# Optimization experiments

Hardware: AMD Instinct MI355X
Metric: run time of the kernel (lower is better)

## Reference

```python
import jax, jax.numpy as jnp
import numpy as np


def _conv1x1(x, W, b):
    # x: (n, c_in, h, w); W: (c_out, c_in); b: (c_out,)
    return jnp.einsum('nchw,oc->nohw', x, W) + b[None, :, None, None]


def setup_inputs() -> dict:
    key = jax.random.key(0)
    ks = jax.random.split(key, 9)
    n, C, h, w = 2, 256, 64, 64
    Ch = C // 2
    s_in = 0.02
    return {
        'feature': jax.random.normal(ks[0], (n, C, h, w), dtype=jnp.float32),
        'Wq': jax.random.normal(ks[1], (Ch, C), dtype=jnp.float32) * s_in,
        'bq': jax.random.normal(ks[2], (Ch,), dtype=jnp.float32) * s_in,
        'Wk': jax.random.normal(ks[3], (Ch, C), dtype=jnp.float32) * s_in,
        'bk': jax.random.normal(ks[4], (Ch,), dtype=jnp.float32) * s_in,
        'Wv': jax.random.normal(ks[5], (Ch, C), dtype=jnp.float32) * s_in,
        'bv': jax.random.normal(ks[6], (Ch,), dtype=jnp.float32) * s_in,
        'Wm': jax.random.normal(ks[7], (C, Ch), dtype=jnp.float32) * s_in,
        'bm': jax.random.normal(ks[8], (C,), dtype=jnp.float32) * s_in,
    }


def reference(feature, Wq, bq, Wk, bk, Wv, bv, Wm, bm):
    n, C, h, w = feature.shape
    Ch = C // 2
    N = n * h * w
    # 1x1 conv projections, then flatten batch+spatial into one sequence dim
    q = _conv1x1(feature, Wq, bq)  # (n, Ch, h, w)
    k = _conv1x1(feature, Wk, bk)
    v = _conv1x1(feature, Wv, bv)
    # NCHW -> NHWC -> (N, Ch), matching torch transpose(1,2).transpose(2,3).reshape
    q = jnp.transpose(q, (0, 2, 3, 1)).reshape(N, Ch)
    k = jnp.transpose(k, (0, 2, 3, 1)).reshape(N, Ch)
    v = jnp.transpose(v, (0, 2, 3, 1)).reshape(N, Ch)
    # scores = k @ q.T (note: torch code uses k as rows, q.T as cols)
    scores = k @ q.T  # (N, N)
    attn = jax.nn.softmax(scores, axis=-1)
    mask = attn @ v  # (N, Ch)
    mask = mask.reshape(n, h, w, Ch)
    # torch transpose chain (2,3)->(1,2)->(2,3): (n,h,w,Ch) -> (n,Ch,w,h)
    mask = jnp.transpose(mask, (0, 3, 2, 1))
    out = _conv1x1(mask, Wm, bm)  # (n, C, w, h); h==w so residual add is valid
    return out + feature
```

## Files before the change

### kernel.cpp

```cpp
#include <hip/hip_runtime.h>
#include <hip/hip_bf16.h>

#define LOG2E 1.44269504088896340736f

typedef __attribute__((ext_vector_type(8))) short short8;
typedef __attribute__((ext_vector_type(4))) float f32x4;
typedef __attribute__((ext_vector_type(2))) unsigned int uint2v;
typedef __attribute__((ext_vector_type(4))) unsigned int uint4v;
typedef unsigned int u32;

__device__ __forceinline__ short f2bf(float f) {
    unsigned u = __builtin_bit_cast(unsigned, f);
    unsigned r = (u + 0x7FFFu + ((u >> 16) & 1u)) >> 16;
    return (short)r;
}

__device__ __forceinline__ float bf2f(short x) {
    unsigned u = ((unsigned)(unsigned short)x) << 16;
    return __builtin_bit_cast(float, u);
}

__device__ __forceinline__ unsigned cvt_pk_bf16(float lo, float hi) {
    unsigned r;
    asm volatile("v_cvt_pk_bf16_f32 %0, %1, %2" : "=v"(r) : "v"(lo), "v"(hi));
    return r;
}

__device__ __forceinline__ float fexp2(float x) {
    float r;
    asm("v_exp_f32 %0, %1" : "=v"(r) : "v"(x));
    return r;
}

__global__ __launch_bounds__(64) void wprep_kernel(
    const float* __restrict__ Wq, const float* __restrict__ bq,
    const float* __restrict__ Wk, const float* __restrict__ bk,
    const float* __restrict__ Wv, const float* __restrict__ bv,
    const float* __restrict__ Wm,
    short* __restrict__ Wb, float* __restrict__ bqkv, short* __restrict__ Wmb)
{
    const int b = blockIdx.x;
    const int t = threadIdx.x;
    if (b < 384) {
        const int mat = b >> 7, row = b & 127;
        const float* src = (mat == 0 ? Wq : mat == 1 ? Wk : Wv) + (size_t)row * 256;
        const float sc = (mat == 1) ? LOG2E : 1.f;
        float4 v = *(const float4*)(src + t * 4);
        uint2v pk;
        pk.x = cvt_pk_bf16(v.x * sc, v.y * sc);
        pk.y = cvt_pk_bf16(v.z * sc, v.w * sc);
        *(uint2v*)(Wb + (size_t)b * 256 + t * 4) = pk;
    } else if (b == 384) {
        for (int e = t; e < 384; e += 64) {
            const int mat = e >> 7;
            const float* bsrc = (mat == 0 ? bq : mat == 1 ? bk : bv);
            bqkv[e] = bsrc[e & 127] * (mat == 1 ? LOG2E : 1.f);
        }
    } else {
        const int row = b - 385;
        float2 v = *(const float2*)(Wm + (size_t)row * 128 + t * 2);
        *(u32*)(Wmb + (size_t)row * 128 + t * 2) = cvt_pk_bf16(v.x, v.y);
    }
}

__global__ __launch_bounds__(256) void proj_kernel(
    const float* __restrict__ feat, const short* __restrict__ Wb,
    const float* __restrict__ bqkv,
    short* __restrict__ Qb, short* __restrict__ Kb, short* __restrict__ VTg)
{
    __shared__ __align__(16) short Xs[16 * 256];
    __shared__ __align__(16) short VTs[128 * 16];
    const int t = threadIdx.x;
    const int blk = blockIdx.x;
    const int ib = blk * 16;
    const int n = ib >> 12;
    const int hw0 = ib & 4095;

    {
        const int r = t & 15, cg = t >> 4;
        const float* fp = feat + (size_t)n * 1048576 + (size_t)(cg * 16) * 4096 + hw0 + r;
        short8 t0, t1;
        #pragma unroll
        for (int ci = 0; ci < 8; ++ci) {
            t0[ci] = f2bf(fp[(size_t)ci * 4096]);
            t1[ci] = f2bf(fp[(size_t)(ci + 8) * 4096]);
        }
        const int sw = (r & 7) << 2;
        *(short8*)(&Xs[r * 256 + ((cg * 2) ^ sw) * 8]) = t0;
        *(short8*)(&Xs[r * 256 + ((cg * 2 + 1) ^ sw) * 8]) = t1;
    }
    __syncthreads();

    const int lane = t & 63;
    const int w = __builtin_amdgcn_readfirstlane(t >> 6);
    const int l15 = lane & 15;
    const int g = lane >> 4;
    const int o0w = w * 96;

    f32x4 acc[6];
    #pragma unroll
    for (int osub = 0; osub < 6; ++osub)
        acc[osub] = *(const f32x4*)(bqkv + o0w + osub * 16 + 4 * g);

    const short* wbase = Wb + (size_t)(o0w + l15) * 256 + g * 8;
    const int xsw = (l15 & 7) << 2;
    #pragma unroll
    for (int kc = 0; kc < 8; ++kc) {
        short8 xf = *(const short8*)(&Xs[l15 * 256 + (((kc * 4 + g) ^ xsw) * 8)]);
        #pragma unroll
        for (int osub = 0; osub < 6; ++osub) {
            short8 wf = *(const short8*)(wbase + (size_t)osub * 16 * 256 + kc * 32);
            acc[osub] = __builtin_amdgcn_mfma_f32_16x16x32_bf16(wf, xf, acc[osub], 0, 0, 0);
        }
    }

    #pragma unroll
    for (int osub = 0; osub < 6; ++osub) {
        const int o0 = o0w + osub * 16;
        const int mat = o0 >> 7;
        const int col = (o0 & 127) + 4 * g;
        if (mat == 0) {
            uint2v pk;
            pk.x = cvt_pk_bf16(acc[osub][0], acc[osub][1]);
            pk.y = cvt_pk_bf16(acc[osub][2], acc[osub][3]);
            *(uint2v*)(Qb + (size_t)(ib + l15) * 128 + col) = pk;
        } else if (mat == 1) {
            uint2v pk;
            pk.x = cvt_pk_bf16(acc[osub][0], acc[osub][1]);
            pk.y = cvt_pk_bf16(acc[osub][2], acc[osub][3]);
            *(uint2v*)(Kb + (size_t)(ib + l15) * 128 + col) = pk;
        } else {
            #pragma unroll
            for (int reg = 0; reg < 4; ++reg)
                VTs[(col + reg) * 16 + l15] = f2bf(acc[osub][reg]);
        }
    }
    __syncthreads();

    {
        const int o = t >> 1, ih = (t & 1) * 8;
        short8 vv = *(const short8*)(&VTs[o * 16 + ih]);
        const int jt = ib >> 5;
        const int u = (ib >> 4) & 1;
        const int g0 = ih >> 2;
        short* vb = VTg + (size_t)jt * 4096 + (o >> 4) * 512 + (o & 15) * 8 + 4 * u;
        uint4v q = __builtin_bit_cast(uint4v, vv);
        uint2v lo; lo.x = q.x; lo.y = q.y;
        uint2v hi; hi.x = q.z; hi.y = q.w;
        *(uint2v*)(vb + g0 * 128) = lo;
        *(uint2v*)(vb + (g0 + 1) * 128) = hi;
    }
}

__global__ __launch_bounds__(256, 2) void attn_kernel(
    const short* __restrict__ Qb, const short* __restrict__ Kb,
    const short* __restrict__ VTg,
    short* __restrict__ Opart, float* __restrict__ Ssb)
{
    __shared__ __align__(16) char smem[32768];

    const int tid = threadIdx.x;
    const int lane = tid & 63;
    const int w = __builtin_amdgcn_readfirstlane(tid >> 6);
    const int l15 = lane & 15;
    const int g = lane >> 4;
    const int blk = blockIdx.x;
    const int ibX = blk >> 3;
    const int jq  = blk & 7;
    const int iw  = ibX * 128 + w * 32;
    const int j0  = jq * 1024;

    short8 kf[2][4];
    #pragma unroll
    for (int iset = 0; iset < 2; ++iset)
        #pragma unroll
        for (int dcq = 0; dcq < 4; ++dcq)
            kf[iset][dcq] = *(const short8*)(Kb + (size_t)(iw + iset * 16 + l15) * 128 + dcq * 32 + g * 8);

    f32x4 O[2][8];
    #pragma unroll
    for (int iset = 0; iset < 2; ++iset)
        #pragma unroll
        for (int dc = 0; dc < 8; ++dc) O[iset][dc] = (f32x4){0.f, 0.f, 0.f, 0.f};
    float s[2] = {0.f, 0.f};

    const short* srcQ0;
    const short* srcQ1;
    {
        int r0 = 4 * w + (lane >> 4), c0 = lane & 15;
        srcQ0 = Qb + (size_t)(j0 + r0) * 128 + (c0 ^ (r0 & 7)) * 8;
        int r1 = 16 + 4 * w + (lane >> 4);
        srcQ1 = Qb + (size_t)(j0 + r1) * 128 + (c0 ^ (r1 & 7)) * 8;
    }

    auto stage = [&](int quarter) {
        char* base = smem + quarter * 8192;
        __builtin_amdgcn_global_load_lds(
            (const __attribute__((address_space(1))) u32*)(const void*)srcQ0,
            (__attribute__((address_space(3))) u32*)(void*)(base + w * 1024), 16, 0, 0);
        __builtin_amdgcn_global_load_lds(
            (const __attribute__((address_space(1))) u32*)(const void*)srcQ1,
            (__attribute__((address_space(3))) u32*)(void*)(base + (4 + w) * 1024), 16, 0, 0);
        srcQ0 += 32 * 128;
        srcQ1 += 32 * 128;
    };

    const short* vp = VTg + (size_t)(jq * 32) * 4096 + lane * 8;
    short8 vA[8], vB[8];
    auto loadV = [&](short8 (&vr)[8]) {
        #pragma unroll
        for (int dc = 0; dc < 8; ++dc)
            vr[dc] = *(const short8*)(vp + dc * 512);
        vp += 4096;
    };

    auto compute32 = [&](const char* Qt, const short8 (&vr)[8]) {
        const int xs = (l15 & 7) << 4;

        f32x4 sv[2][2];
        #pragma unroll
        for (int jh = 0; jh < 2; ++jh)
            #pragma unroll
            for (int iset = 0; iset < 2; ++iset)
                sv[jh][iset] = (f32x4){-16.f, -16.f, -16.f, -16.f};

        __builtin_amdgcn_s_setprio(1);
        #pragma unroll
        for (int dcq = 0; dcq < 4; ++dcq) {
            short8 qa0 = *(const short8*)(Qt + ((l15 * 256 + dcq * 64 + g * 16) ^ xs));
            short8 qa1 = *(const short8*)(Qt + (((l15 + 16) * 256 + dcq * 64 + g * 16) ^ xs));
            sv[0][0] = __builtin_amdgcn_mfma_f32_16x16x32_bf16(qa0, kf[0][dcq], sv[0][0], 0, 0, 0);
            sv[0][1] = __builtin_amdgcn_mfma_f32_16x16x32_bf16(qa0, kf[1][dcq], sv[0][1], 0, 0, 0);
            sv[1][0] = __builtin_amdgcn_mfma_f32_16x16x32_bf16(qa1, kf[0][dcq], sv[1][0], 0, 0, 0);
            sv[1][1] = __builtin_amdgcn_mfma_f32_16x16x32_bf16(qa1, kf[1][dcq], sv[1][1], 0, 0, 0);
        }
        __builtin_amdgcn_s_setprio(0);

        short8 pf[2];
        #pragma unroll
        for (int iset = 0; iset < 2; ++iset) {
            float p0[4], p1[4], ps = 0.f;
            #pragma unroll
            for (int e = 0; e < 4; ++e) {
                p0[e] = fexp2(sv[0][iset][e]);
                p1[e] = fexp2(sv[1][iset][e]);
                ps += p0[e] + p1[e];
            }
            s[iset] += ps;
            uint4v pk;
            pk.x = cvt_pk_bf16(p0[0], p0[1]);
            pk.y = cvt_pk_bf16(p0[2], p0[3]);
            pk.z = cvt_pk_bf16(p1[0], p1[1]);
            pk.w = cvt_pk_bf16(p1[2], p1[3]);
            pf[iset] = __builtin_bit_cast(short8, pk);
        }

        __builtin_amdgcn_s_setprio(1);
        #pragma unroll
        for (int dc = 0; dc < 8; ++dc) {
            O[0][dc] = __builtin_amdgcn_mfma_f32_16x16x32_bf16(vr[dc], pf[0], O[0][dc], 0, 0, 0);
            O[1][dc] = __builtin_amdgcn_mfma_f32_16x16x32_bf16(vr[dc], pf[1], O[1][dc], 0, 0, 0);
        }
        __builtin_amdgcn_s_setprio(0);
    };

    stage(0);
    stage(1);
    loadV(vA);
    __syncthreads();
    for (int tt = 0; tt < 32; tt += 2) {
        if (tt + 2 < 32) {
            stage((tt + 2) & 3);
            stage((tt + 3) & 3);
        }
        loadV(vB);
        compute32(smem + (tt & 3) * 8192, vA);
        if (tt + 2 < 32) loadV(vA);
        compute32(smem + ((tt + 1) & 3) * 8192, vB);
        __syncthreads();
    }

    #pragma unroll
    for (int iset = 0; iset < 2; ++iset) {
        const int i = iw + iset * 16 + l15;
        #pragma unroll
        for (int dc = 0; dc < 8; ++dc) {
            uint2v pk;
            pk.x = cvt_pk_bf16(O[iset][dc][0], O[iset][dc][1]);
            pk.y = cvt_pk_bf16(O[iset][dc][2], O[iset][dc][3]);
            *(uint2v*)(Opart + ((size_t)i * 8 + jq) * 128 + dc * 16 + 4 * g) = pk;
        }
        Ssb[(i * 8 + jq) * 4 + g] = s[iset];
    }
}

__global__ __launch_bounds__(256, 4) void epi_kernel(
    const short* __restrict__ Opart, const float* __restrict__ Ssb,
    const short* __restrict__ Wmb, const float* __restrict__ bm,
    const float* __restrict__ feat, float* __restrict__ out)
{
    __shared__ __align__(16) short Ms[16 * 128];
    const int t = threadIdx.x;
    const int blk = blockIdx.x;
    const int yt = blk & 3;
    const int x = (blk >> 2) & 63;
    const int n = blk >> 8;
    const int y0 = yt * 16;

    {
        const int r = t >> 4, c = t & 15;
        const int i = n * 4096 + (y0 + r) * 64 + x;
        float acc8[8] = {0.f, 0.f, 0.f, 0.f, 0.f, 0.f, 0.f, 0.f};
        #pragma unroll
        for (int q = 0; q < 8; ++q) {
            short8 o = *(const short8*)(Opart + ((size_t)i * 8 + q) * 128 + c * 8);
            #pragma unroll
            for (int e = 0; e < 8; ++e) acc8[e] += bf2f(o[e]);
        }
        float2 s2 = *(const float2*)(Ssb + (size_t)i * 32 + c * 2);
        float tp = s2.x + s2.y;
        tp += __shfl_xor(tp, 1);
        tp += __shfl_xor(tp, 2);
        tp += __shfl_xor(tp, 4);
        tp += __shfl_xor(tp, 8);
        const float inv = 1.f / tp;
        uint4v pk;
        pk.x = cvt_pk_bf16(acc8[0] * inv, acc8[1] * inv);
        pk.y = cvt_pk_bf16(acc8[2] * inv, acc8[3] * inv);
        pk.z = cvt_pk_bf16(acc8[4] * inv, acc8[5] * inv);
        pk.w = cvt_pk_bf16(acc8[6] * inv, acc8[7] * inv);
        *(short8*)(&Ms[r * 128 + ((c ^ ((r & 7) << 1)) * 8)]) =
            __builtin_bit_cast(short8, pk);
    }
    __syncthreads();

    const int lane = t & 63;
    const int w = __builtin_amdgcn_readfirstlane(t >> 6);
    const int l15 = lane & 15;
    const int g = lane >> 4;
    const int c0 = w * 64;

    short8 bf[4];
    const int msw = (l15 & 7) << 1;
    #pragma unroll
    for (int dcq = 0; dcq < 4; ++dcq)
        bf[dcq] = *(const short8*)(&Ms[l15 * 128 + (((dcq * 4 + g) ^ msw) * 8)]);

    f32x4 acc[4];
    #pragma unroll
    for (int ct = 0; ct < 4; ++ct)
        acc[ct] = *(const f32x4*)(bm + c0 + ct * 16 + 4 * g);

    const short* wbase = Wmb + (size_t)(c0 + l15) * 128 + g * 8;
    #pragma unroll
    for (int dcq = 0; dcq < 4; ++dcq) {
        #pragma unroll
        for (int ct = 0; ct < 4; ++ct) {
            short8 wf = *(const short8*)(wbase + (size_t)ct * 16 * 128 + dcq * 32);
            acc[ct] = __builtin_amdgcn_mfma_f32_16x16x32_bf16(wf, bf[dcq], acc[ct], 0, 0, 0);
        }
    }

    #pragma unroll
    for (int ct = 0; ct < 4; ++ct) {
        #pragma unroll
        for (int reg = 0; reg < 4; ++reg) {
            const int c = c0 + ct * 16 + 4 * g + reg;
            const size_t oidx = (((size_t)(n * 256 + c) * 64 + x) * 64) + y0 + l15;
            out[oidx] = acc[ct][reg] + feat[oidx];
        }
    }
}

extern "C" void kernel_launch(void* const* d_in, const int* in_sizes, int n_in,
                              void* d_out, int out_size, void* d_ws, size_t ws_size,
                              hipStream_t stream) {
    const float* feat = (const float*)d_in[0];
    const float* Wq = (const float*)d_in[1];
    const float* bq = (const float*)d_in[2];
    const float* Wk = (const float*)d_in[3];
    const float* bk = (const float*)d_in[4];
    const float* Wv = (const float*)d_in[5];
    const float* bv = (const float*)d_in[6];
    const float* Wm = (const float*)d_in[7];
    const float* bm = (const float*)d_in[8];
    float* out = (float*)d_out;

    short* Qb = (short*)d_ws;
    short* Kb = Qb + 8192 * 128;
    short* VTg = Kb + 8192 * 128;
    short* Opart = VTg + 8192 * 128;
    float* Ssb = (float*)(Opart + (size_t)8 * 8192 * 128);
    float* bqkv = Ssb + (size_t)8192 * 32;
    short* Wb = (short*)(bqkv + 384);
    short* Wmb = Wb + 384 * 256;

    hipLaunchKernelGGL(wprep_kernel, dim3(641), dim3(64), 0, stream,
                       Wq, bq, Wk, bk, Wv, bv, Wm, Wb, bqkv, Wmb);
    hipLaunchKernelGGL(proj_kernel, dim3(512), dim3(256), 0, stream,
                       feat, Wb, bqkv, Qb, Kb, VTg);
    hipLaunchKernelGGL(attn_kernel, dim3(512), dim3(256), 0, stream,
                       Qb, Kb, VTg, Opart, Ssb);
    hipLaunchKernelGGL(epi_kernel, dim3(512), dim3(256), 0, stream,
                       Opart, Ssb, Wmb, bm, feat, out);
}
```

Before: 76.91 us.

## Split attention key range across waves with LDS reduction, drop shared Q staging

Each workgroup now covers 32 query rows, and its four waves each handle a different 256-column slice of the key/value range instead of each wave owning different rows. Q and V fragments are loaded straight from global memory into registers, replacing the LDS-staged Q pipeline with its per-iteration barriers. The partial outputs and sums are then reduced across waves through LDS before the bf16 partials are written. The grid grows to 2048 blocks for more parallelism, at the cost of an LDS reduction step and uncoalesced direct global Q loads with no double buffering.

```diff
diff --git a/kernel.cpp b/kernel.cpp
--- a/kernel.cpp
+++ b/kernel.cpp
@@ -157,7 +157,8 @@
     const short* __restrict__ VTg,
     short* __restrict__ Opart, float* __restrict__ Ssb)
 {
-    __shared__ __align__(16) char smem[32768];
+    __shared__ float Obuf[4][2][16][132];
+    __shared__ float Sbuf[4][2][16][4];
 
     const int tid = threadIdx.x;
     const int lane = tid & 63;
@@ -167,8 +168,8 @@
     const int blk = blockIdx.x;
     const int ibX = blk >> 3;
     const int jq  = blk & 7;
-    const int iw  = ibX * 128 + w * 32;
-    const int j0  = jq * 1024;
+    const int iw  = ibX * 32;
+    const int j0  = jq * 1024 + w * 256;
 
     short8 kf[2][4];
     #pragma unroll
@@ -184,39 +185,34 @@
         for (int dc = 0; dc < 8; ++dc) O[iset][dc] = (f32x4){0.f, 0.f, 0.f, 0.f};
     float s[2] = {0.f, 0.f};
 
-    const short* srcQ0;
-    const short* srcQ1;
-    {
-        int r0 = 4 * w + (lane >> 4), c0 = lane & 15;
-        srcQ0 = Qb + (size_t)(j0 + r0) * 128 + (c0 ^ (r0 & 7)) * 8;
-        int r1 = 16 + 4 * w + (lane >> 4);
-        srcQ1 = Qb + (size_t)(j0 + r1) * 128 + (c0 ^ (r1 & 7)) * 8;
-    }
-
-    auto stage = [&](int quarter) {
-        char* base = smem + quarter * 8192;
-        __builtin_amdgcn_global_load_lds(
-            (const __attribute__((address_space(1))) u32*)(const void*)srcQ0,
-            (__attribute__((address_space(3))) u32*)(void*)(base + w * 1024), 16, 0, 0);
-        __builtin_amdgcn_global_load_lds(
-            (const __attribute__((address_space(1))) u32*)(const void*)srcQ1,
-            (__attribute__((address_space(3))) u32*)(void*)(base + (4 + w) * 1024), 16, 0, 0);
-        srcQ0 += 32 * 128;
-        srcQ1 += 32 * 128;
+    const short* qp0 = Qb + (size_t)(j0 + l15) * 128 + g * 8;
+    const short* qp1 = qp0 + 16 * 128;
+    const short* vp0 = VTg + (size_t)(j0 >> 5) * 4096 + lane * 8;
+    const short* vp4 = vp0 + 4 * 512;
+
+    short8 qa[2][4], vr[8];
+    auto loadQ = [&]() {
+        #pragma unroll
+        for (int dcq = 0; dcq < 4; ++dcq) {
+            qa[0][dcq] = *(const short8*)(qp0 + dcq * 32);
+            qa[1][dcq] = *(const short8*)(qp1 + dcq * 32);
+        }
+        qp0 += 32 * 128;
+        qp1 += 32 * 128;
     };
-
-    const short* vp = VTg + (size_t)(jq * 32) * 4096 + lane * 8;
-    short8 vA[8], vB[8];
-    auto loadV = [&](short8 (&vr)[8]) {
-        #pragma unroll
-        for (int dc = 0; dc < 8; ++dc)
-            vr[dc] = *(const short8*)(vp + dc * 512);
-        vp += 4096;
+    auto loadV = [&]() {
+        #pragma unroll
+        for (int dc = 0; dc < 4; ++dc) {
+            vr[dc]     = *(const short8*)(vp0 + dc * 512);
+            vr[4 + dc] = *(const short8*)(vp4 + dc * 512);
+        }
+        vp0 += 4096;
+        vp4 += 4096;
     };
 
-    auto compute32 = [&](const char* Qt, const short8 (&vr)[8]) {
-        const int xs = (l15 & 7) << 4;
-
+    loadQ();
+    loadV();
+    for (int t = 0; t < 8; ++t) {
         f32x4 sv[2][2];
         #pragma unroll
         for (int jh = 0; jh < 2; ++jh)
@@ -227,14 +223,14 @@
         __builtin_amdgcn_s_setprio(1);
         #pragma unroll
         for (int dcq = 0; dcq < 4; ++dcq) {
-            short8 qa0 = *(const short8*)(Qt + ((l15 * 256 + dcq * 64 + g * 16) ^ xs));
-            short8 qa1 = *(const short8*)(Qt + (((l15 + 16) * 256 + dcq * 64 + g * 16) ^ xs));
-            sv[0][0] = __builtin_amdgcn_mfma_f32_16x16x32_bf16(qa0, kf[0][dcq], sv[0][0], 0, 0, 0);
-            sv[0][1] = __builtin_amdgcn_mfma_f32_16x16x32_bf16(qa0, kf[1][dcq], sv[0][1], 0, 0, 0);
-            sv[1][0] = __builtin_amdgcn_mfma_f32_16x16x32_bf16(qa1, kf[0][dcq], sv[1][0], 0, 0, 0);
-            sv[1][1] = __builtin_amdgcn_mfma_f32_16x16x32_bf16(qa1, kf[1][dcq], sv[1][1], 0, 0, 0);
+            sv[0][0] = __builtin_amdgcn_mfma_f32_16x16x32_bf16(qa[0][dcq], kf[0][dcq], sv[0][0], 0, 0, 0);
+            sv[0][1] = __builtin_amdgcn_mfma_f32_16x16x32_bf16(qa[0][dcq], kf[1][dcq], sv[0][1], 0, 0, 0);
+            sv[1][0] = __builtin_amdgcn_mfma_f32_16x16x32_bf16(qa[1][dcq], kf[0][dcq], sv[1][0], 0, 0, 0);
+            sv[1][1] = __builtin_amdgcn_mfma_f32_16x16x32_bf16(qa[1][dcq], kf[1][dcq], sv[1][1], 0, 0, 0);
         }
         __builtin_amdgcn_s_setprio(0);
+
+        if (t < 7) loadQ();
 
         short8 pf[2];
         #pragma unroll
@@ -262,35 +258,61 @@
             O[1][dc] = __builtin_amdgcn_mfma_f32_16x16x32_bf16(vr[dc], pf[1], O[1][dc], 0, 0, 0);
         }
         __builtin_amdgcn_s_setprio(0);
-    };
-
-    stage(0);
-    stage(1);
-    loadV(vA);
+
+        if (t < 7) loadV();
+    }
+
+    #pragma unroll
+    for (int iset = 0; iset < 2; ++iset) {
+        #pragma unroll
+        for (int dc = 0; dc < 8; ++dc)
+            *(f32x4*)(&Obuf[w][iset][l15][dc * 16 + 4 * g]) = O[iset][dc];
+        Sbuf[w][iset][l15][g] = s[iset];
+    }
     __syncthreads();
-    for (int tt = 0; tt < 32; tt += 2) {
-        if (tt + 2 < 32) {
-            stage((tt + 2) & 3);
-            stage((tt + 3) & 3);
-        }
-        loadV(vB);
-        compute32(smem + (tt & 3) * 8192, vA);
-        if (tt + 2 < 32) loadV(vA);
-        compute32(smem + ((tt + 1) & 3) * 8192, vB);
-        __syncthreads();
-    }
-
-    #pragma unroll
-    for (int iset = 0; iset < 2; ++iset) {
-        const int i = iw + iset * 16 + l15;
-        #pragma unroll
-        for (int dc = 0; dc < 8; ++dc) {
-            uint2v pk;
-            pk.x = cvt_pk_bf16(O[iset][dc][0], O[iset][dc][1]);
-            pk.y = cvt_pk_bf16(O[iset][dc][2], O[iset][dc][3]);
-            *(uint2v*)(Opart + ((size_t)i * 8 + jq) * 128 + dc * 16 + 4 * g) = pk;
-        }
-        Ssb[(i * 8 + jq) * 4 + g] = s[iset];
+
+    {
+        const int r = tid >> 3;
+        const int dch = (tid & 7) * 16;
+        const int iset = r >> 4, lr = r & 15;
+        const int i = iw + r;
+
+        float acc[16];
+        #pragma unroll
+        for (int e = 0; e < 16; ++e) acc[e] = 0.f;
+        #pragma unroll
+        for (int ww = 0; ww < 4; ++ww) {
+            #pragma unroll
+            for (int e4 = 0; e4 < 4; ++e4) {
+                f32x4 v = *(const f32x4*)(&Obuf[ww][iset][lr][dch + e4 * 4]);
+                acc[e4 * 4 + 0] += v[0];
+                acc[e4 * 4 + 1] += v[1];
+                acc[e4 * 4 + 2] += v[2];
+                acc[e4 * 4 + 3] += v[3];
+            }
+        }
+        uint4v pk0, pk1;
+        pk0.x = cvt_pk_bf16(acc[0], acc[1]);
+        pk0.y = cvt_pk_bf16(acc[2], acc[3]);
+        pk0.z = cvt_pk_bf16(acc[4], acc[5]);
+        pk0.w = cvt_pk_bf16(acc[6], acc[7]);
+        pk1.x = cvt_pk_bf16(acc[8], acc[9]);
+        pk1.y = cvt_pk_bf16(acc[10], acc[11]);
+        pk1.z = cvt_pk_bf16(acc[12], acc[13]);
+        pk1.w = cvt_pk_bf16(acc[14], acc[15]);
+        short* op = Opart + ((size_t)i * 8 + jq) * 128 + dch;
+        *(uint4v*)(op) = pk0;
+        *(uint4v*)(op + 8) = pk1;
+
+        if ((tid & 7) == 0) {
+            f32x4 T = {0.f, 0.f, 0.f, 0.f};
+            #pragma unroll
+            for (int ww = 0; ww < 4; ++ww) {
+                f32x4 sv4 = *(const f32x4*)(&Sbuf[ww][iset][lr][0]);
+                T[0] += sv4[0]; T[1] += sv4[1]; T[2] += sv4[2]; T[3] += sv4[3];
+            }
+            *(f32x4*)(Ssb + ((size_t)i * 8 + jq) * 4) = T;
+        }
     }
 }
 
@@ -399,7 +421,7 @@
                        Wq, bq, Wk, bk, Wv, bv, Wm, Wb, bqkv, Wmb);
     hipLaunchKernelGGL(proj_kernel, dim3(512), dim3(256), 0, stream,
                        feat, Wb, bqkv, Qb, Kb, VTg);
-    hipLaunchKernelGGL(attn_kernel, dim3(512), dim3(256), 0, stream,
+    hipLaunchKernelGGL(attn_kernel, dim3(2048), dim3(256), 0, stream,
                        Qb, Kb, VTg, Opart, Ssb);
     hipLaunchKernelGGL(epi_kernel, dim3(512), dim3(256), 0, stream,
                        Opart, Ssb, Wmb, bm, feat, out);
```

Measured after the change: 118.2 us. 53.7% more time.
